# Kernel tuning notes

Hardware: AMD Instinct MI355X
Metric: run time of the kernel (lower is better)

## Reference

```python
import jax, jax.numpy as jnp
import numpy as np

KERNEL_SIZE = 3

def setup_inputs() -> dict:
    key = jax.random.key(0)
    k1, k2, k3, k4, k5 = jax.random.split(key, 5)
    B, L, D, K = 4, 4096, 1024, KERNEL_SIZE
    x = jax.random.normal(k1, (B, L, D), dtype=jnp.float32)
    # depthwise conv: torch weight shape (D, 1, K) -> store as (D, K)
    fan_dw = 1.0 / np.sqrt(1 * K)
    w_dw = jax.random.uniform(k2, (D, K), dtype=jnp.float32, minval=-fan_dw, maxval=fan_dw)
    b_dw = jax.random.uniform(k3, (D,), dtype=jnp.float32, minval=-fan_dw, maxval=fan_dw)
    # pointwise conv: torch weight shape (D, D, 1) -> store as (D_out, D_in)
    fan_pw = 1.0 / np.sqrt(D * 1)
    w_pw = jax.random.uniform(k4, (D, D), dtype=jnp.float32, minval=-fan_pw, maxval=fan_pw)
    b_pw = jax.random.uniform(k5, (D,), dtype=jnp.float32, minval=-fan_pw, maxval=fan_pw)
    return {"x": x, "w_dw": w_dw, "b_dw": b_dw, "w_pw": w_pw, "b_pw": b_pw}

def _causal_dw_pw(x, w_dw, b_dw, w_pw, b_pw):
    # x: (B, L, D); causal left-pad by K-1 along L
    K = w_dw.shape[1]
    L = x.shape[1]
    xp = jnp.pad(x, ((0, 0), (K - 1, 0), (0, 0)))  # (B, L+K-1, D)
    # depthwise: y[b,l,d] = sum_k xp[b,l+k,d] * w_dw[d,k]
    y = sum(xp[:, k:k + L, :] * w_dw[:, k] for k in range(K)) + b_dw
    # pointwise 1x1 conv: mix channels
    return jnp.einsum('bld,ed->ble', y, w_pw) + b_pw

def reference(x, w_dw, b_dw, w_pw, b_pw):
    return _causal_dw_pw(x, w_dw, b_dw, w_pw, b_pw)
```

## Files before the change

### kernel.cpp

```cpp
#include <hip/hip_runtime.h>
#include <hip/hip_bf16.h>
#include <stdint.h>

#define B_SZ   4
#define L_SEQ  4096
#define D_DIM  1024
#define M_TOT  (B_SZ * L_SEQ)

typedef __bf16 bf16;
typedef __attribute__((ext_vector_type(8))) __bf16 bf16x8;
typedef __attribute__((ext_vector_type(4))) float   f32x4;

#define GLOAD_LDS16(g, l)                                                     \
  __builtin_amdgcn_global_load_lds(                                           \
      (const __attribute__((address_space(1))) void*)(g),                     \
      (__attribute__((address_space(3))) void*)(l), 16, 0, 0)

__global__ __launch_bounds__(256) void dw_bf16_kernel(
    const float* __restrict__ x, const float* __restrict__ w_dw,
    const float* __restrict__ b_dw, bf16* __restrict__ y,
    const float* __restrict__ w_pw, bf16* __restrict__ wpwb) {
  const int t = threadIdx.x;
  if (blockIdx.x >= B_SZ * (L_SEQ / 16)) {
    int i = ((blockIdx.x - B_SZ * (L_SEQ / 16)) * 256 + t) * 8;
    float4 a = *(const float4*)(w_pw + i);
    float4 b = *(const float4*)(w_pw + i + 4);
    union { bf16 h[8]; int4 v; } r;
    r.h[0] = (bf16)a.x; r.h[1] = (bf16)a.y; r.h[2] = (bf16)a.z; r.h[3] = (bf16)a.w;
    r.h[4] = (bf16)b.x; r.h[5] = (bf16)b.y; r.h[6] = (bf16)b.z; r.h[7] = (bf16)b.w;
    *(int4*)(wpwb + i) = r.v;
    return;
  }
  const int b  = blockIdx.x >> 8;
  const int l0 = (blockIdx.x & 255) * 16;
  const int d0 = t * 4;
  const float* xb = x + (size_t)b * L_SEQ * D_DIM + d0;
  bf16*        yb = y + (size_t)b * L_SEQ * D_DIM + d0;

  float4 xr[18];
  const float4 zero = make_float4(0.f, 0.f, 0.f, 0.f);
  xr[0] = (l0 >= 2) ? *(const float4*)(xb + (size_t)(l0 - 2) * D_DIM) : zero;
  xr[1] = (l0 >= 1) ? *(const float4*)(xb + (size_t)(l0 - 1) * D_DIM) : zero;
#pragma unroll
  for (int j = 0; j < 16; ++j)
    xr[j + 2] = *(const float4*)(xb + (size_t)(l0 + j) * D_DIM);

  const float* wp = w_dw + d0 * 3;
  float4 wa = *(const float4*)(wp);
  float4 wb = *(const float4*)(wp + 4);
  float4 wc = *(const float4*)(wp + 8);
  float4 bv = *(const float4*)(b_dw + d0);

#pragma unroll
  for (int j = 0; j < 16; ++j) {
    float4 x2 = xr[j], x1 = xr[j + 1], x0 = xr[j + 2];
    float a0 = fmaf(x2.x, wa.x, fmaf(x1.x, wa.y, fmaf(x0.x, wa.z, bv.x)));
    float a1 = fmaf(x2.y, wa.w, fmaf(x1.y, wb.x, fmaf(x0.y, wb.y, bv.y)));
    float a2 = fmaf(x2.z, wb.z, fmaf(x1.z, wb.w, fmaf(x0.z, wc.x, bv.z)));
    float a3 = fmaf(x2.w, wc.y, fmaf(x1.w, wc.z, fmaf(x0.w, wc.w, bv.w)));
    union { bf16 h[4]; int2 v; } o;
    o.h[0] = (bf16)a0; o.h[1] = (bf16)a1; o.h[2] = (bf16)a2; o.h[3] = (bf16)a3;
    *(int2*)(yb + (size_t)(l0 + j) * D_DIM) = o.v;
  }
}

#define EP_ROWP 68
#define SB  __builtin_amdgcn_s_barrier()
#define SCB __builtin_amdgcn_sched_barrier(0)
#define VM(N) asm volatile("s_waitcnt vmcnt(" #N ")" ::: "memory")

__global__ __launch_bounds__(1024, 4) void gemm256_kernel(
    const bf16* __restrict__ A,
    const bf16* __restrict__ Bm,
    const float* __restrict__ bias, float* __restrict__ C) {
  __shared__ __align__(16) char smem[131072];

  const int t    = threadIdx.x;
  const int m0   = blockIdx.x * 256;
  const int n0   = blockIdx.y * 256;
  const int lane = t & 63;
  const int wv   = t >> 6;
  const int wm4  = wv >> 2;
  const int wn4  = wv & 3;
  const int lrow = lane & 15;
  const int q    = lane >> 4;

  const unsigned cx    = (((unsigned)q ^ (((unsigned)lrow >> 1) & 3)) << 4);
  const unsigned baseA = (unsigned)((wm4 * 64 + lrow) * 64) + cx;
  const unsigned baseB = (unsigned)((wn4 * 64 + lrow) * 64) + cx;

  const int grow = t >> 2;
  const int gc   = (t & 3) ^ ((grow >> 1) & 3);
  const bf16* aSrc = A  + (size_t)(m0 + grow) * D_DIM + gc * 8;
  const bf16* bSrc = Bm + (size_t)(n0 + grow) * D_DIM + gc * 8;
  const unsigned wbase = (unsigned)(wv * 1024);

  auto stage = [&](int s) {
    const size_t k0 = (size_t)s * 32;
    unsigned as_ = (unsigned)((s & 3) * 16384) + wbase;
    GLOAD_LDS16(aSrc + k0, smem + as_);
    GLOAD_LDS16(bSrc + k0, smem + as_ + 65536);
  };

  f32x4 acc[4][4] = {};

  auto body = [&](int s, bool do_stage) {
    SB;
    const char* Ab = smem + (size_t)((s & 3) * 16384);
    const char* Bb = Ab + 65536;
    bf16x8 af[4], bf4[4];
#pragma unroll
    for (int j = 0; j < 4; ++j) bf4[j] = *(const bf16x8*)(Bb + baseB + j * 1024);
#pragma unroll
    for (int i = 0; i < 4; ++i) af[i]  = *(const bf16x8*)(Ab + baseA + i * 1024);
    if (do_stage) stage(s + 3);
    SCB;
    __builtin_amdgcn_s_setprio(1);
#pragma unroll
    for (int i = 0; i < 4; ++i)
#pragma unroll
      for (int j = 0; j < 4; ++j)
        acc[i][j] = __builtin_amdgcn_mfma_f32_16x16x32_bf16(af[i], bf4[j], acc[i][j], 0, 0, 0);
    __builtin_amdgcn_s_setprio(0);
    SCB;
  };

  stage(0); stage(1); stage(2);

  for (int s = 0; s < 30; ++s) { VM(4); body(s, s <= 28); }
  VM(2); body(30, false);
  VM(0); body(31, false);

  __syncthreads();
  float* ep = (float*)smem + (size_t)wv * (16 * EP_ROWP);

  float bvj[4];
#pragma unroll
  for (int j = 0; j < 4; ++j) bvj[j] = bias[n0 + wn4 * 64 + j * 16 + lrow];

#pragma unroll
  for (int i = 0; i < 4; ++i) {
#pragma unroll
    for (int j = 0; j < 4; ++j)
#pragma unroll
      for (int r = 0; r < 4; ++r)
        ep[(q * 4 + r) * EP_ROWP + j * 16 + lrow] = acc[i][j][r] + bvj[j];
#pragma unroll
    for (int it2 = 0; it2 < 4; ++it2) {
      int flat = it2 * 64 + lane;
      int row  = flat >> 4;
      int c16  = flat & 15;
      float4 v = *(const float4*)(ep + row * EP_ROWP + c16 * 4);
      int gm = m0 + wm4 * 64 + i * 16 + row;
      int gn = n0 + wn4 * 64 + c16 * 4;
      *(float4*)(C + (size_t)gm * D_DIM + gn) = v;
    }
  }
}

__global__ __launch_bounds__(256) void fallback_kernel(
    const float* __restrict__ x, const float* __restrict__ w_dw,
    const float* __restrict__ b_dw, const float* __restrict__ w_pw,
    const float* __restrict__ b_pw, float* __restrict__ out) {
  __shared__ float ys[D_DIM];
  const int m = blockIdx.x;
  const int l = m & (L_SEQ - 1);
  const int t = threadIdx.x;
  const float* xr = x + (size_t)m * D_DIM;
#pragma unroll
  for (int c = 0; c < 4; ++c) {
    int d = t + c * 256;
    float a = fmaf(xr[d], w_dw[d * 3 + 2], b_dw[d]);
    if (l >= 1) a = fmaf(xr[d - D_DIM], w_dw[d * 3 + 1], a);
    if (l >= 2) a = fmaf(xr[d - 2 * D_DIM], w_dw[d * 3 + 0], a);
    ys[d] = a;
  }
  __syncthreads();
#pragma unroll
  for (int c = 0; c < 4; ++c) {
    int e = t + c * 256;
    const float* wr = w_pw + (size_t)e * D_DIM;
    float a = b_pw[e];
    for (int d = 0; d < D_DIM; ++d) a = fmaf(ys[d], wr[d], a);
    out[(size_t)m * D_DIM + e] = a;
  }
}

extern "C" void kernel_launch(void* const* d_in, const int* in_sizes, int n_in,
                              void* d_out, int out_size, void* d_ws, size_t ws_size,
                              hipStream_t stream) {
  (void)in_sizes; (void)n_in; (void)out_size;
  const float* x    = (const float*)d_in[0];
  const float* w_dw = (const float*)d_in[1];
  const float* b_dw = (const float*)d_in[2];
  const float* w_pw = (const float*)d_in[3];
  const float* b_pw = (const float*)d_in[4];
  float* out = (float*)d_out;

  const size_t y_elems = (size_t)M_TOT * D_DIM;
  const size_t w_elems = (size_t)D_DIM * D_DIM;
  const size_t need = (y_elems + w_elems) * sizeof(bf16);

  if (ws_size >= need) {
    bf16* y    = (bf16*)d_ws;
    bf16* wpwb = (bf16*)d_ws + y_elems;
    const int dw_blocks  = B_SZ * (L_SEQ / 16);
    const int cvt_blocks = (D_DIM * D_DIM / 8) / 256;
    dw_bf16_kernel<<<dw_blocks + cvt_blocks, 256, 0, stream>>>(x, w_dw, b_dw, y, w_pw, wpwb);
    dim3 grid(M_TOT / 256, D_DIM / 256);
    gemm256_kernel<<<grid, 1024, 0, stream>>>(y, wpwb, b_pw, out);
  } else {
    fallback_kernel<<<M_TOT, 256, 0, stream>>>(x, w_dw, b_dw, w_pw, b_pw, out);
  }
}
```

Baseline: 154.1 us.

## Load GEMM B fragments directly into registers and shrink LDS to double-buffered A

The B (weight) operand is no longer staged through LDS. Each wave loads its B fragments straight from global memory into registers, double-buffered across k-steps. The A ring drops from four LDS stages to two, which cuts the shared-memory allocation and the LDS read traffic for B. In exchange, pipelining depth for A falls, B global loads are no longer shared between waves (redundant fetches served by L2), and register pressure rises.

```diff
diff --git a/kernel.cpp b/kernel.cpp
--- a/kernel.cpp
+++ b/kernel.cpp
@@ -73,7 +73,7 @@
     const bf16* __restrict__ A,
     const bf16* __restrict__ Bm,
     const float* __restrict__ bias, float* __restrict__ C) {
-  __shared__ __align__(16) char smem[131072];
+  __shared__ __align__(16) char smem[69632];
 
   const int t    = threadIdx.x;
   const int m0   = blockIdx.x * 256;
@@ -87,51 +87,58 @@
 
   const unsigned cx    = (((unsigned)q ^ (((unsigned)lrow >> 1) & 3)) << 4);
   const unsigned baseA = (unsigned)((wm4 * 64 + lrow) * 64) + cx;
-  const unsigned baseB = (unsigned)((wn4 * 64 + lrow) * 64) + cx;
 
   const int grow = t >> 2;
   const int gc   = (t & 3) ^ ((grow >> 1) & 3);
-  const bf16* aSrc = A  + (size_t)(m0 + grow) * D_DIM + gc * 8;
-  const bf16* bSrc = Bm + (size_t)(n0 + grow) * D_DIM + gc * 8;
+  const bf16* aSrc = A + (size_t)(m0 + grow) * D_DIM + gc * 8;
   const unsigned wbase = (unsigned)(wv * 1024);
 
-  auto stage = [&](int s) {
-    const size_t k0 = (size_t)s * 32;
-    unsigned as_ = (unsigned)((s & 3) * 16384) + wbase;
-    GLOAD_LDS16(aSrc + k0, smem + as_);
-    GLOAD_LDS16(bSrc + k0, smem + as_ + 65536);
+  const bf16* bPtr = Bm + (size_t)(n0 + wn4 * 64 + lrow) * D_DIM + q * 8;
+
+  auto stage_a = [&](int s) {
+    GLOAD_LDS16(aSrc + (size_t)s * 32, smem + (unsigned)((s & 1) * 16384) + wbase);
   };
 
   f32x4 acc[4][4] = {};
-
-  auto body = [&](int s, bool do_stage) {
+  bf16x8 bA[4], bB[4];
+
+#define LOADB(dst, s) do {                                                    \
+    _Pragma("unroll")                                                         \
+    for (int j = 0; j < 4; ++j)                                               \
+      dst[j] = *(const bf16x8*)(bPtr + (size_t)j * 16 * D_DIM + (size_t)(s) * 32); \
+  } while (0)
+
+  auto body = [&](int s, bf16x8* bcur, bf16x8* bnxt, int mode) {
     SB;
-    const char* Ab = smem + (size_t)((s & 3) * 16384);
-    const char* Bb = Ab + 65536;
-    bf16x8 af[4], bf4[4];
-#pragma unroll
-    for (int j = 0; j < 4; ++j) bf4[j] = *(const bf16x8*)(Bb + baseB + j * 1024);
-#pragma unroll
-    for (int i = 0; i < 4; ++i) af[i]  = *(const bf16x8*)(Ab + baseA + i * 1024);
-    if (do_stage) stage(s + 3);
-    SCB;
+    const char* Ab = smem + (size_t)((s & 1) * 16384);
+    bf16x8 af[4];
+#pragma unroll
+    for (int i = 0; i < 4; ++i) af[i] = *(const bf16x8*)(Ab + baseA + i * 1024);
+    if (mode == 0) { stage_a(s + 1); SCB; LOADB((*(bf16x8(*)[4])bnxt), s + 1); SCB; VM(5); }
+    else if (mode == 1) { LOADB((*(bf16x8(*)[4])bnxt), s + 1); SCB; VM(4); }
+    else { VM(0); }
     __builtin_amdgcn_s_setprio(1);
 #pragma unroll
     for (int i = 0; i < 4; ++i)
 #pragma unroll
       for (int j = 0; j < 4; ++j)
-        acc[i][j] = __builtin_amdgcn_mfma_f32_16x16x32_bf16(af[i], bf4[j], acc[i][j], 0, 0, 0);
+        acc[i][j] = __builtin_amdgcn_mfma_f32_16x16x32_bf16(af[i], bcur[j], acc[i][j], 0, 0, 0);
     __builtin_amdgcn_s_setprio(0);
     SCB;
   };
 
-  stage(0); stage(1); stage(2);
-
-  for (int s = 0; s < 30; ++s) { VM(4); body(s, s <= 28); }
-  VM(2); body(30, false);
-  VM(0); body(31, false);
-
-  __syncthreads();
+  stage_a(0); SCB;
+  LOADB(bA, 0); SCB;
+
+#pragma unroll 1
+  for (int s = 0; s < 30; s += 2) {
+    VM(4); body(s, bA, bB, 0);
+    VM(4); body(s + 1, bB, bA, 0);
+  }
+  VM(4); body(30, bA, bB, 0);
+  VM(4); body(31, bB, bA, 2);
+
+  SB;
   float* ep = (float*)smem + (size_t)wv * (16 * EP_ROWP);
 
   float bvj[4];
@@ -156,6 +163,7 @@
       *(float4*)(C + (size_t)gm * D_DIM + gn) = v;
     }
   }
+#undef LOADB
 }
 
 __global__ __launch_bounds__(256) void fallback_kernel(
```

Result: slower. 197.7 us (+28.2%).

## Fuse depthwise conv into GEMM A-tile producer, drop bf16 intermediate

Applied to the files above, without the earlier changes.

The depthwise causal conv is now computed inside the GEMM: each block loads fp32 x rows (plus two previous rows), applies the conv, converts to bf16 and writes the A tile straight into LDS, software-pipelined with the B-tile async loads. This removes the separate conv kernel and the round trip of the bf16 y tensor through global memory. The tile shape changes from 256x256 with 1024 threads to 256x128 with 512 threads, and LDS use is halved. The cost is recomputing the conv once per N tile (8 times per row) and re-reading x, including the two halo rows, from global memory for every N tile.

```diff
diff --git a/kernel.cpp b/kernel.cpp
--- a/kernel.cpp
+++ b/kernel.cpp
@@ -16,105 +16,123 @@
       (const __attribute__((address_space(1))) void*)(g),                     \
       (__attribute__((address_space(3))) void*)(l), 16, 0, 0)
 
-__global__ __launch_bounds__(256) void dw_bf16_kernel(
-    const float* __restrict__ x, const float* __restrict__ w_dw,
-    const float* __restrict__ b_dw, bf16* __restrict__ y,
+__global__ __launch_bounds__(256) void cvt_kernel(
     const float* __restrict__ w_pw, bf16* __restrict__ wpwb) {
-  const int t = threadIdx.x;
-  if (blockIdx.x >= B_SZ * (L_SEQ / 16)) {
-    int i = ((blockIdx.x - B_SZ * (L_SEQ / 16)) * 256 + t) * 8;
-    float4 a = *(const float4*)(w_pw + i);
-    float4 b = *(const float4*)(w_pw + i + 4);
-    union { bf16 h[8]; int4 v; } r;
-    r.h[0] = (bf16)a.x; r.h[1] = (bf16)a.y; r.h[2] = (bf16)a.z; r.h[3] = (bf16)a.w;
-    r.h[4] = (bf16)b.x; r.h[5] = (bf16)b.y; r.h[6] = (bf16)b.z; r.h[7] = (bf16)b.w;
-    *(int4*)(wpwb + i) = r.v;
-    return;
-  }
-  const int b  = blockIdx.x >> 8;
-  const int l0 = (blockIdx.x & 255) * 16;
-  const int d0 = t * 4;
-  const float* xb = x + (size_t)b * L_SEQ * D_DIM + d0;
-  bf16*        yb = y + (size_t)b * L_SEQ * D_DIM + d0;
-
-  float4 xr[18];
-  const float4 zero = make_float4(0.f, 0.f, 0.f, 0.f);
-  xr[0] = (l0 >= 2) ? *(const float4*)(xb + (size_t)(l0 - 2) * D_DIM) : zero;
-  xr[1] = (l0 >= 1) ? *(const float4*)(xb + (size_t)(l0 - 1) * D_DIM) : zero;
-#pragma unroll
-  for (int j = 0; j < 16; ++j)
-    xr[j + 2] = *(const float4*)(xb + (size_t)(l0 + j) * D_DIM);
-
-  const float* wp = w_dw + d0 * 3;
-  float4 wa = *(const float4*)(wp);
-  float4 wb = *(const float4*)(wp + 4);
-  float4 wc = *(const float4*)(wp + 8);
-  float4 bv = *(const float4*)(b_dw + d0);
-
-#pragma unroll
-  for (int j = 0; j < 16; ++j) {
-    float4 x2 = xr[j], x1 = xr[j + 1], x0 = xr[j + 2];
-    float a0 = fmaf(x2.x, wa.x, fmaf(x1.x, wa.y, fmaf(x0.x, wa.z, bv.x)));
-    float a1 = fmaf(x2.y, wa.w, fmaf(x1.y, wb.x, fmaf(x0.y, wb.y, bv.y)));
-    float a2 = fmaf(x2.z, wb.z, fmaf(x1.z, wb.w, fmaf(x0.z, wc.x, bv.z)));
-    float a3 = fmaf(x2.w, wc.y, fmaf(x1.w, wc.z, fmaf(x0.w, wc.w, bv.w)));
-    union { bf16 h[4]; int2 v; } o;
-    o.h[0] = (bf16)a0; o.h[1] = (bf16)a1; o.h[2] = (bf16)a2; o.h[3] = (bf16)a3;
-    *(int2*)(yb + (size_t)(l0 + j) * D_DIM) = o.v;
-  }
+  int i = (blockIdx.x * 256 + threadIdx.x) * 8;
+  float4 a = *(const float4*)(w_pw + i);
+  float4 b = *(const float4*)(w_pw + i + 4);
+  union { bf16 h[8]; int4 v; } r;
+  r.h[0] = (bf16)a.x; r.h[1] = (bf16)a.y; r.h[2] = (bf16)a.z; r.h[3] = (bf16)a.w;
+  r.h[4] = (bf16)b.x; r.h[5] = (bf16)b.y; r.h[6] = (bf16)b.z; r.h[7] = (bf16)b.w;
+  *(int4*)(wpwb + i) = r.v;
 }
 
 #define EP_ROWP 68
 #define SB  __builtin_amdgcn_s_barrier()
 #define SCB __builtin_amdgcn_sched_barrier(0)
 #define VM(N) asm volatile("s_waitcnt vmcnt(" #N ")" ::: "memory")
-
-__global__ __launch_bounds__(1024, 4) void gemm256_kernel(
-    const bf16* __restrict__ A,
-    const bf16* __restrict__ Bm,
+#define LGKM0 asm volatile("s_waitcnt lgkmcnt(0)" ::: "memory")
+
+__global__ __launch_bounds__(512, 2) void fused_gemm(
+    const float* __restrict__ x, const float* __restrict__ w_dw,
+    const float* __restrict__ b_dw, const bf16* __restrict__ Bm,
     const float* __restrict__ bias, float* __restrict__ C) {
-  __shared__ __align__(16) char smem[131072];
+  __shared__ __align__(16) char smem[65536];
 
   const int t    = threadIdx.x;
   const int m0   = blockIdx.x * 256;
-  const int n0   = blockIdx.y * 256;
+  const int n0   = blockIdx.y * 128;
   const int lane = t & 63;
   const int wv   = t >> 6;
-  const int wm4  = wv >> 2;
-  const int wn4  = wv & 3;
+  const int wm4  = wv >> 1;
+  const int wn2  = wv & 1;
   const int lrow = lane & 15;
   const int q    = lane >> 4;
 
-  const unsigned cx    = (((unsigned)q ^ (((unsigned)lrow >> 1) & 3)) << 4);
-  const unsigned baseA = (unsigned)((wm4 * 64 + lrow) * 64) + cx;
-  const unsigned baseB = (unsigned)((wn4 * 64 + lrow) * 64) + cx;
-
-  const int grow = t >> 2;
-  const int gc   = (t & 3) ^ ((grow >> 1) & 3);
-  const bf16* aSrc = A  + (size_t)(m0 + grow) * D_DIM + gc * 8;
-  const bf16* bSrc = Bm + (size_t)(n0 + grow) * D_DIM + gc * 8;
-  const unsigned wbase = (unsigned)(wv * 1024);
-
-  auto stage = [&](int s) {
-    const size_t k0 = (size_t)s * 32;
-    unsigned as_ = (unsigned)((s & 3) * 16384) + wbase;
-    GLOAD_LDS16(aSrc + k0, smem + as_);
-    GLOAD_LDS16(bSrc + k0, smem + as_ + 65536);
+  const unsigned cxr   = (((unsigned)q ^ (((unsigned)lrow >> 1) & 3)) << 4);
+  const unsigned baseA = (unsigned)((wm4 * 64 + lrow) * 64) + cxr;
+  const unsigned baseB = (unsigned)((wn2 * 64 + lrow) * 64) + cxr;
+
+  const int rt = t >> 2;
+  const int c  = t & 3;
+  const unsigned cS = (unsigned)(c ^ ((rt >> 1) & 3));
+
+  const bf16* bSrc = Bm + (size_t)(n0 + rt) * D_DIM + (c ^ ((rt >> 1) & 3)) * 8;
+  const unsigned wvbase = (unsigned)(wv * 1024);
+
+  const int mrow0 = m0 + rt;
+  const int mrow1 = m0 + 128 + rt;
+  const int lloc  = mrow0 & (L_SEQ - 1);
+  const bool z2 = (lloc < 2), z1 = (lloc < 1);
+  const float* xp0 = x + (size_t)mrow0 * D_DIM + c * 8;
+  const float* xp1 = x + (size_t)mrow1 * D_DIM + c * 8;
+  const float* xp0m2 = z2 ? xp0 : (xp0 - 2 * D_DIM);
+  const float* xp0m1 = z1 ? xp0 : (xp0 - 1 * D_DIM);
+
+  float xbuf[2][3][8];
+  float wbuf[24], bbuf[8];
+
+  auto stageB = [&](int s) {
+    GLOAD_LDS16(bSrc + (size_t)s * 32,
+                smem + 32768u + (unsigned)((s & 3) * 8192) + wvbase);
+  };
+
+  auto issue_xwb = [&](int sl) {
+    const int k8 = sl * 32;
+    *(float4*)&xbuf[0][0][0] = *(const float4*)(xp0m2 + k8);
+    *(float4*)&xbuf[0][0][4] = *(const float4*)(xp0m2 + k8 + 4);
+    *(float4*)&xbuf[0][1][0] = *(const float4*)(xp0m1 + k8);
+    *(float4*)&xbuf[0][1][4] = *(const float4*)(xp0m1 + k8 + 4);
+    *(float4*)&xbuf[0][2][0] = *(const float4*)(xp0 + k8);
+    *(float4*)&xbuf[0][2][4] = *(const float4*)(xp0 + k8 + 4);
+    *(float4*)&xbuf[1][0][0] = *(const float4*)(xp1 - 2 * D_DIM + k8);
+    *(float4*)&xbuf[1][0][4] = *(const float4*)(xp1 - 2 * D_DIM + k8 + 4);
+    *(float4*)&xbuf[1][1][0] = *(const float4*)(xp1 - 1 * D_DIM + k8);
+    *(float4*)&xbuf[1][1][4] = *(const float4*)(xp1 - 1 * D_DIM + k8 + 4);
+    *(float4*)&xbuf[1][2][0] = *(const float4*)(xp1 + k8);
+    *(float4*)&xbuf[1][2][4] = *(const float4*)(xp1 + k8 + 4);
+    const float* wp = w_dw + (size_t)(k8 + c * 8) * 3;
+#pragma unroll
+    for (int v = 0; v < 6; ++v)
+      *(float4*)&wbuf[v * 4] = *(const float4*)(wp + v * 4);
+    *(float4*)&bbuf[0] = *(const float4*)(b_dw + k8 + c * 8);
+    *(float4*)&bbuf[4] = *(const float4*)(b_dw + k8 + c * 8 + 4);
+  };
+
+  auto conv_store = [&](int sl) {
+    const unsigned abase = (unsigned)((sl & 1) * 16384);
+#pragma unroll
+    for (int G = 0; G < 2; ++G) {
+      union { bf16 h[8]; int4 v; } o;
+#pragma unroll
+      for (int c8 = 0; c8 < 8; ++c8) {
+        float xm2 = xbuf[G][0][c8], xm1 = xbuf[G][1][c8], xm0 = xbuf[G][2][c8];
+        if (G == 0) { xm2 = z2 ? 0.f : xm2; xm1 = z1 ? 0.f : xm1; }
+        o.h[c8] = (bf16)fmaf(xm2, wbuf[c8 * 3],
+                     fmaf(xm1, wbuf[c8 * 3 + 1],
+                       fmaf(xm0, wbuf[c8 * 3 + 2], bbuf[c8])));
+      }
+      *(int4*)(smem + abase + (unsigned)((G * 128 + rt) * 64) + cS * 16) = o.v;
+    }
   };
 
   f32x4 acc[4][4] = {};
 
-  auto body = [&](int s, bool do_stage) {
+  auto body = [&](int s, int mode) {
+    if (mode == 0) stageB(s + 3);
+    const char* Ab = (const char*)smem + (size_t)((s & 1) * 16384);
+    const char* Bb = (const char*)smem + 32768 + (size_t)((s & 3) * 8192);
+    bf16x8 af[4], bf4[4];
+#pragma unroll
+    for (int j = 0; j < 4; ++j) bf4[j] = *(const bf16x8*)(Bb + baseB + j * 1024);
+#pragma unroll
+    for (int i = 0; i < 4; ++i) af[i]  = *(const bf16x8*)(Ab + baseA + i * 1024);
+    if (mode == 0) { VM(1); } else { VM(0); }
+    if (mode <= 2) conv_store(s + 1);
+    if (mode <= 1) issue_xwb(s + 2);
+    LGKM0;
+    SCB;
     SB;
-    const char* Ab = smem + (size_t)((s & 3) * 16384);
-    const char* Bb = Ab + 65536;
-    bf16x8 af[4], bf4[4];
-#pragma unroll
-    for (int j = 0; j < 4; ++j) bf4[j] = *(const bf16x8*)(Bb + baseB + j * 1024);
-#pragma unroll
-    for (int i = 0; i < 4; ++i) af[i]  = *(const bf16x8*)(Ab + baseA + i * 1024);
-    if (do_stage) stage(s + 3);
-    SCB;
     __builtin_amdgcn_s_setprio(1);
 #pragma unroll
     for (int i = 0; i < 4; ++i)
@@ -125,18 +143,26 @@
     SCB;
   };
 
-  stage(0); stage(1); stage(2);
-
-  for (int s = 0; s < 30; ++s) { VM(4); body(s, s <= 28); }
-  VM(2); body(30, false);
-  VM(0); body(31, false);
-
-  __syncthreads();
+  stageB(0); stageB(1); stageB(2);
+  issue_xwb(0);
+  VM(0);
+  conv_store(0);
+  issue_xwb(1);
+  LGKM0;
+  SB;
+
+#pragma unroll 1
+  for (int s = 0; s < 29; ++s) body(s, 0);
+  body(29, 1);
+  body(30, 2);
+  body(31, 3);
+
+  SB;
   float* ep = (float*)smem + (size_t)wv * (16 * EP_ROWP);
 
   float bvj[4];
 #pragma unroll
-  for (int j = 0; j < 4; ++j) bvj[j] = bias[n0 + wn4 * 64 + j * 16 + lrow];
+  for (int j = 0; j < 4; ++j) bvj[j] = bias[n0 + wn2 * 64 + j * 16 + lrow];
 
 #pragma unroll
   for (int i = 0; i < 4; ++i) {
@@ -152,7 +178,7 @@
       int c16  = flat & 15;
       float4 v = *(const float4*)(ep + row * EP_ROWP + c16 * 4);
       int gm = m0 + wm4 * 64 + i * 16 + row;
-      int gn = n0 + wn4 * 64 + c16 * 4;
+      int gn = n0 + wn2 * 64 + c16 * 4;
       *(float4*)(C + (size_t)gm * D_DIM + gn) = v;
     }
   }
@@ -197,18 +223,14 @@
   const float* b_pw = (const float*)d_in[4];
   float* out = (float*)d_out;
 
-  const size_t y_elems = (size_t)M_TOT * D_DIM;
   const size_t w_elems = (size_t)D_DIM * D_DIM;
-  const size_t need = (y_elems + w_elems) * sizeof(bf16);
+  const size_t need = w_elems * sizeof(bf16);
 
   if (ws_size >= need) {
-    bf16* y    = (bf16*)d_ws;
-    bf16* wpwb = (bf16*)d_ws + y_elems;
-    const int dw_blocks  = B_SZ * (L_SEQ / 16);
-    const int cvt_blocks = (D_DIM * D_DIM / 8) / 256;
-    dw_bf16_kernel<<<dw_blocks + cvt_blocks, 256, 0, stream>>>(x, w_dw, b_dw, y, w_pw, wpwb);
-    dim3 grid(M_TOT / 256, D_DIM / 256);
-    gemm256_kernel<<<grid, 1024, 0, stream>>>(y, wpwb, b_pw, out);
+    bf16* wpwb = (bf16*)d_ws;
+    cvt_kernel<<<(D_DIM * D_DIM / 8) / 256, 256, 0, stream>>>(w_pw, wpwb);
+    dim3 grid(M_TOT / 256, D_DIM / 128);
+    fused_gemm<<<grid, 512, 0, stream>>>(x, w_dw, b_dw, wpwb, b_pw, out);
   } else {
     fallback_kernel<<<M_TOT, 256, 0, stream>>>(x, w_dw, b_dw, w_pw, b_pw, out);
   }
```

New measurement: 231.3 us. 1.5x slower.
